# Kernel tuning notes

Measured on AMD Instinct MI355X. Metric: run time of the kernel, lower is better.

The kernel has to match this reference:

```python
import jax, jax.numpy as jnp
import numpy as np
from jax import lax

N, M, B = 512, 1024, 1024  # signal dim, atoms, batch (batch==m required by X = W @ Gamma)
POWER_ITER = 100
IHT_ITER = 50


def setup_inputs() -> dict:
    key = jax.random.key(0)
    k1, k2 = jax.random.split(key)
    Y = jax.random.normal(k1, (B, N), dtype=jnp.float32)
    W = jax.random.normal(k2, (N, M), dtype=jnp.float32)
    return {"Y": Y, "W": W, "K": 64}


def power_method(W):
    # 100 iterations of X <- X W^T W / ||.||; returns last pre-normalization norm
    # (approx largest eigenvalue of W^T W), matching PowerMethod in the source.
    X0 = jax.random.normal(jax.random.key(42), (1, W.shape[1]), dtype=W.dtype)

    def body(i, carry):
        X, _ = carry
        X2 = (X @ W.T) @ W          # [1, m]
        nm = jnp.linalg.norm(X2)
        return (X2 / nm, nm)

    _, nm = lax.fori_loop(0, POWER_ITER, body, (X0, jnp.asarray(1.0, W.dtype)))
    return nm


def hard_threshold_k(G, K):
    # keep entries strictly larger (in abs) than the (K+1)-th largest per row
    a = jnp.sort(jnp.abs(G), axis=1)[:, ::-1]   # descending per row
    T = a[:, K][:, None]                          # [B, 1]
    return G * (jnp.abs(G) > T).astype(G.dtype)


def reference(Y, W, K):
    # NormDict: column-normalize the dictionary
    W = W / jnp.linalg.norm(W, axis=0)
    c = power_method(W)
    eta = 1.0 / c
    Yn = jnp.linalg.norm(Y)

    # IHT sparse coding
    Gamma = hard_threshold_k(Y @ (eta * W), K)     # [B, m]
    residual = Gamma @ W.T - Y                      # [B, n]

    def step(carry, _):
        Gamma, residual = carry
        Gamma = hard_threshold_k(Gamma - eta * (residual @ W), K)
        residual = Gamma @ W.T - Y
        return (Gamma, residual), jnp.linalg.norm(residual) / Yn

    (Gamma, residual), norms = lax.scan(step, (Gamma, residual), None, length=IHT_ITER)

    X = W @ Gamma  # [n, m] @ [B, m] -> requires B == m, as in the torch source
    return X, Gamma, norms
```

## Files before the change

kernel.cpp:

```cpp
#include <hip/hip_runtime.h>


#define DEV __device__ __forceinline__

constexpr int Nd = 512;
constexpr int Md = 1024;
constexpr int Bd = 1024;
constexpr int Ksp = 64;
constexpr int IHT = 50;

DEV float wave_reduce_f(float v) {
#pragma unroll
  for (int off = 32; off > 0; off >>= 1) v += __shfl_down(v, off);
  return v;
}
DEV double wave_reduce_d(double v) {
#pragma unroll
  for (int off = 32; off > 0; off >>= 1) v += __shfl_down(v, off);
  return v;
}
DEV float rfl_f(float v) {
  return __uint_as_float(__builtin_amdgcn_readfirstlane(__float_as_uint(v)));
}

__global__ void k_zero(double* dacc) {
  int t = threadIdx.x;
  if (t < 51) dacc[t] = 0.0;
}

__global__ __launch_bounds__(256) void k_colnorm(const float* __restrict__ W,
                                                 float* __restrict__ cnorm) {
  int col = blockIdx.x * 256 + threadIdx.x;
  double ss = 0.0;
  for (int i = 0; i < Nd; ++i) {
    float w = W[(size_t)i * Md + col];
    ss = fma((double)w, (double)w, ss);
  }
  cnorm[col] = (float)sqrt(ss);
}

__global__ __launch_bounds__(256) void k_normalize(const float* __restrict__ W,
                                                   const float* __restrict__ cnorm,
                                                   float* __restrict__ Wn) {
  int idx = blockIdx.x * 256 + threadIdx.x;
  Wn[idx] = W[idx] / cnorm[idx & (Md - 1)];
}

__global__ __launch_bounds__(256) void k_yn2(const float* __restrict__ Y,
                                             double* __restrict__ dacc) {
  double s = 0.0;
  for (int i = blockIdx.x * 256 + threadIdx.x; i < Bd * Nd; i += gridDim.x * 256) {
    float y = Y[i];
    s = fma((double)y, (double)y, s);
  }
  s = wave_reduce_d(s);
  __shared__ double red[4];
  int lane = threadIdx.x & 63, wid = threadIdx.x >> 6;
  if (lane == 0) red[wid] = s;
  __syncthreads();
  if (threadIdx.x == 0) atomicAdd(&dacc[0], red[0] + red[1] + red[2] + red[3]);
}

template <int BM, int BN, int TN>
__global__ __launch_bounds__(256) void k_gemm_t(const float* __restrict__ A, int lda, int ta,
                                                const float* __restrict__ B, int ldb, int tb,
                                                float* __restrict__ C, int ldc, int Kd,
                                                float scale) {
  constexpr int AE = 32 * BM / 256;
  constexpr int BE = 32 * BN / 256;
  __shared__ __align__(16) float As[32][BM + 4];
  __shared__ __align__(16) float Bs[32][BN + 4];
  const int tid = threadIdx.x;
  const int tx = tid % (BN / TN), ty = tid / (BN / TN);
  const int m0 = blockIdx.y * BM, n0 = blockIdx.x * BN;
  float ra[AE], rb[BE];
  float acc[4][TN];
#pragma unroll
  for (int i = 0; i < 4; ++i)
#pragma unroll
    for (int j = 0; j < TN; ++j) acc[i][j] = 0.f;

  auto loadA = [&](int k0) {
    if (!ta) {
      const int c = tid & 31, r0 = tid >> 5;
#pragma unroll
      for (int i = 0; i < AE; ++i)
        ra[i] = A[(size_t)(m0 + r0 + i * 8) * lda + (k0 + c)];
    } else {
      const int r = tid % BM, c0 = tid / BM;
#pragma unroll
      for (int i = 0; i < AE; ++i)
        ra[i] = A[(size_t)(k0 + c0 + i * (256 / BM)) * lda + (m0 + r)];
    }
  };
  auto storeA = [&]() {
    if (!ta) {
      const int c = tid & 31, r0 = tid >> 5;
#pragma unroll
      for (int i = 0; i < AE; ++i) As[c][r0 + i * 8] = ra[i];
    } else {
      const int r = tid % BM, c0 = tid / BM;
#pragma unroll
      for (int i = 0; i < AE; ++i) As[c0 + i * (256 / BM)][r] = ra[i];
    }
  };
  auto loadB = [&](int k0) {
    if (!tb) {
      const int c = tid % BN, r0 = tid / BN;
#pragma unroll
      for (int i = 0; i < BE; ++i)
        rb[i] = B[(size_t)(k0 + r0 + i * (256 / BN)) * ldb + (n0 + c)];
    } else {
      const int r = tid & 31, c0 = tid >> 5;
#pragma unroll
      for (int i = 0; i < BE; ++i)
        rb[i] = B[(size_t)(n0 + c0 + i * 8) * ldb + (k0 + r)];
    }
  };
  auto storeB = [&]() {
    if (!tb) {
      const int c = tid % BN, r0 = tid / BN;
#pragma unroll
      for (int i = 0; i < BE; ++i) Bs[r0 + i * (256 / BN)][c] = rb[i];
    } else {
      const int r = tid & 31, c0 = tid >> 5;
#pragma unroll
      for (int i = 0; i < BE; ++i) Bs[r][c0 + i * 8] = rb[i];
    }
  };

  loadA(0);
  loadB(0);
  storeA();
  storeB();
  __syncthreads();
  for (int k0 = 0; k0 < Kd; k0 += 32) {
    const bool more = (k0 + 32) < Kd;
    if (more) { loadA(k0 + 32); loadB(k0 + 32); }
#pragma unroll
    for (int kk = 0; kk < 32; ++kk) {
      const float4 a4 = *(const float4*)&As[kk][ty * 4];
      const float aa[4] = {a4.x, a4.y, a4.z, a4.w};
      float bb[TN];
      if constexpr (TN == 4) {
        const float4 b4 = *(const float4*)&Bs[kk][tx * 4];
        bb[0] = b4.x; bb[1] = b4.y; bb[2] = b4.z; bb[3] = b4.w;
      } else {
        const float2 b2 = *(const float2*)&Bs[kk][tx * 2];
        bb[0] = b2.x; bb[1] = b2.y;
      }
#pragma unroll
      for (int i = 0; i < 4; ++i)
#pragma unroll
        for (int j = 0; j < TN; ++j) acc[i][j] = fmaf(aa[i], bb[j], acc[i][j]);
    }
    if (more) {
      __syncthreads();
      storeA();
      storeB();
      __syncthreads();
    }
  }
#pragma unroll
  for (int i = 0; i < 4; ++i) {
    if constexpr (TN == 4) {
      float4 o;
      o.x = acc[i][0] * scale; o.y = acc[i][1] * scale;
      o.z = acc[i][2] * scale; o.w = acc[i][3] * scale;
      *(float4*)&C[(size_t)(m0 + ty * 4 + i) * ldc + n0 + tx * 4] = o;
    } else {
      float2 o;
      o.x = acc[i][0] * scale; o.y = acc[i][1] * scale;
      *(float2*)&C[(size_t)(m0 + ty * 4 + i) * ldc + n0 + tx * 2] = o;
    }
  }
}

DEV float erfinv_xla(float x) {
  float w = -log1pf(-x * x);
  float p;
  if (w < 5.0f) {
    w = w - 2.5f;
    p = 2.81022636e-08f;
    p = fmaf(p, w, 3.43273939e-07f);
    p = fmaf(p, w, -3.5233877e-06f);
    p = fmaf(p, w, -4.39150654e-06f);
    p = fmaf(p, w, 0.00021858087f);
    p = fmaf(p, w, -0.00125372503f);
    p = fmaf(p, w, -0.00417768164f);
    p = fmaf(p, w, 0.246640727f);
    p = fmaf(p, w, 1.50140941f);
  } else {
    w = sqrtf(w) - 3.0f;
    p = -0.000200214257f;
    p = fmaf(p, w, 0.000100950558f);
    p = fmaf(p, w, 0.00134934322f);
    p = fmaf(p, w, -0.00367342844f);
    p = fmaf(p, w, 0.00573950773f);
    p = fmaf(p, w, -0.0076224613f);
    p = fmaf(p, w, 0.00943887047f);
    p = fmaf(p, w, 1.00167406f);
    p = fmaf(p, w, 2.83297682f);
  }
  return p * x;
}

#define TF_ROUND(r)                                  \
  {                                                  \
    x0 += x1;                                        \
    x1 = (x1 << (r)) | (x1 >> (32 - (r)));           \
    x1 ^= x0;                                        \
  }

__global__ void k_x0(float* __restrict__ X0) {
  unsigned i = threadIdx.x;
  unsigned x0 = i, x1 = i + 512u;
  const unsigned ks0 = 0u, ks1 = 42u, ks2 = 0x1BD11BDAu ^ 42u;
  x0 += ks0; x1 += ks1;
  TF_ROUND(13) TF_ROUND(15) TF_ROUND(26) TF_ROUND(6)  x0 += ks1; x1 += ks2 + 1u;
  TF_ROUND(17) TF_ROUND(29) TF_ROUND(16) TF_ROUND(24) x0 += ks2; x1 += ks0 + 2u;
  TF_ROUND(13) TF_ROUND(15) TF_ROUND(26) TF_ROUND(6)  x0 += ks0; x1 += ks1 + 3u;
  TF_ROUND(17) TF_ROUND(29) TF_ROUND(16) TF_ROUND(24) x0 += ks1; x1 += ks2 + 4u;
  TF_ROUND(13) TF_ROUND(15) TF_ROUND(26) TF_ROUND(6)  x0 += ks2; x1 += ks0 + 5u;
  const float lo = -0.99999994f;
  const float sqrt2 = 1.41421356237f;
  {
    float f = __uint_as_float((x0 >> 9) | 0x3f800000u) - 1.0f;
    float u = fmaxf(lo, f * 2.0f + lo);
    X0[i] = sqrt2 * erfinv_xla(u);
  }
  {
    float f = __uint_as_float((x1 >> 9) | 0x3f800000u) - 1.0f;
    float u = fmaxf(lo, f * 2.0f + lo);
    X0[i + 512] = sqrt2 * erfinv_xla(u);
  }
}

__global__ __launch_bounds__(256) void k_z0(const float* __restrict__ X0,
                                            const float* __restrict__ Wn,
                                            float* __restrict__ vout) {
  const int lane = threadIdx.x & 63, wid = threadIdx.x >> 6;
  const int row = blockIdx.x * 4 + wid;
  const float4* wr = (const float4*)(Wn + (size_t)row * Md);
  const float4* x4 = (const float4*)X0;
  float s = 0.f;
#pragma unroll
  for (int e = 0; e < 4; ++e) {
    const float4 w4 = wr[lane + e * 64];
    const float4 xx = x4[lane + e * 64];
    s = fmaf(w4.x, xx.x, s); s = fmaf(w4.y, xx.y, s);
    s = fmaf(w4.z, xx.z, s); s = fmaf(w4.w, xx.w, s);
  }
  s = wave_reduce_f(s);
  if (lane == 0) vout[row] = s;
}

__global__ __launch_bounds__(256) void k_pmv(const float* __restrict__ Mmat,
                                             const float* __restrict__ vin,
                                             float* __restrict__ vout, float scale) {
  const int lane = threadIdx.x & 63, wid = threadIdx.x >> 6;
  const int row = blockIdx.x * 4 + wid;
  const float4* mr = (const float4*)(Mmat + (size_t)row * Nd);
  const float4* v4 = (const float4*)vin;
  float s = 0.f;
#pragma unroll
  for (int e = 0; e < 2; ++e) {
    const float4 m4 = mr[lane + e * 64];
    const float4 xx = v4[lane + e * 64];
    s = fmaf(m4.x, xx.x, s); s = fmaf(m4.y, xx.y, s);
    s = fmaf(m4.z, xx.z, s); s = fmaf(m4.w, xx.w, s);
  }
  s = wave_reduce_f(s);
  if (lane == 0) vout[row] = s * scale;
}

__global__ __launch_bounds__(512) void k_pfinal(const float* __restrict__ v99,
                                                const float* __restrict__ v100,
                                                float* __restrict__ cbuf) {
  __shared__ double r99[8], r100[8];
  const int t = threadIdx.x, lane = t & 63, wid = t >> 6;
  double a = (double)v99[t]; a *= a;
  double b = (double)v100[t]; b *= b;
  a = wave_reduce_d(a);
  b = wave_reduce_d(b);
  if (lane == 0) { r99[wid] = a; r100[wid] = b; }
  __syncthreads();
  if (t == 0) {
    double n99 = 0.0, n100 = 0.0;
    for (int i = 0; i < 8; ++i) { n99 += r99[i]; n100 += r100[i]; }
    float c = (float)(8.0 * sqrt(n100 / n99));
    cbuf[0] = c;
    cbuf[1] = 1.0f / c;
  }
}

__global__ __launch_bounds__(256) void k_iht_all(
    const float* __restrict__ Q, const float* __restrict__ YW,
    const float* __restrict__ cbuf, float* __restrict__ gdense,
    double* __restrict__ normacc) {
  __shared__ float u[Md];
  __shared__ float yws[Md];
  __shared__ float sval[Ksp];
  __shared__ int sidx[Ksp];
  __shared__ unsigned histbuf[2][4][256];
  __shared__ unsigned wred[4];
  __shared__ unsigned sel_need, sel_prefix;
  __shared__ double dred[4];
  __shared__ int scnt;

  const int t = threadIdx.x;
  const int b = blockIdx.x;
  const int lane = t & 63, wv = t >> 6;
  const float eta = cbuf[1];
  const float4 yw = ((const float4*)(YW + (size_t)b * Md))[t];
  ((float4*)yws)[t] = yw;
#pragma unroll
  for (int e = 0; e < 8; ++e) ((unsigned*)histbuf)[t + e * 256] = 0u;
  const float* Qt = Q + t * 4;

  for (int it = -1; it < IHT; ++it) {
    if (it >= 0) {
      const int cnt = scnt;
      float4 p = make_float4(0.f, 0.f, 0.f, 0.f);
      int k = 0;
      for (; k + 8 <= cnt; k += 8) {
#define GROW(j)                                                        \
        const int id##j = __builtin_amdgcn_readfirstlane(sidx[k + j]); \
        const float g##j = rfl_f(sval[k + j]);                         \
        const float4 q##j = *(const float4*)(Qt + (size_t)id##j * Md);
        GROW(0) GROW(1) GROW(2) GROW(3) GROW(4) GROW(5) GROW(6) GROW(7)
#undef GROW
        p.x = fmaf(g0, q0.x, p.x); p.x = fmaf(g1, q1.x, p.x);
        p.x = fmaf(g2, q2.x, p.x); p.x = fmaf(g3, q3.x, p.x);
        p.x = fmaf(g4, q4.x, p.x); p.x = fmaf(g5, q5.x, p.x);
        p.x = fmaf(g6, q6.x, p.x); p.x = fmaf(g7, q7.x, p.x);
        p.y = fmaf(g0, q0.y, p.y); p.y = fmaf(g1, q1.y, p.y);
        p.y = fmaf(g2, q2.y, p.y); p.y = fmaf(g3, q3.y, p.y);
        p.y = fmaf(g4, q4.y, p.y); p.y = fmaf(g5, q5.y, p.y);
        p.y = fmaf(g6, q6.y, p.y); p.y = fmaf(g7, q7.y, p.y);
        p.z = fmaf(g0, q0.z, p.z); p.z = fmaf(g1, q1.z, p.z);
        p.z = fmaf(g2, q2.z, p.z); p.z = fmaf(g3, q3.z, p.z);
        p.z = fmaf(g4, q4.z, p.z); p.z = fmaf(g5, q5.z, p.z);
        p.z = fmaf(g6, q6.z, p.z); p.z = fmaf(g7, q7.z, p.z);
        p.w = fmaf(g0, q0.w, p.w); p.w = fmaf(g1, q1.w, p.w);
        p.w = fmaf(g2, q2.w, p.w); p.w = fmaf(g3, q3.w, p.w);
        p.w = fmaf(g4, q4.w, p.w); p.w = fmaf(g5, q5.w, p.w);
        p.w = fmaf(g6, q6.w, p.w); p.w = fmaf(g7, q7.w, p.w);
      }
      for (; k < cnt; ++k) {
        const int id = __builtin_amdgcn_readfirstlane(sidx[k]);
        const float g = rfl_f(sval[k]);
        const float4 q = *(const float4*)(Qt + (size_t)id * Md);
        p.x = fmaf(g, q.x, p.x); p.y = fmaf(g, q.y, p.y);
        p.z = fmaf(g, q.z, p.z); p.w = fmaf(g, q.w, p.w);
      }
      ((float4*)u)[t] = p;
      __syncthreads();
      if (it >= 1) {
        double part = 0.0;
        if (t < cnt) {
          const int id = sidx[t];
          part = (double)sval[t] * ((double)u[id] - 2.0 * (double)yws[id]);
        }
        part = wave_reduce_d(part);
        if (lane == 0) dred[wv] = part;
      }
      __syncthreads();
      if (it >= 1 && t == 0)
        atomicAdd(&normacc[it - 1], dred[0] + dred[1] + dred[2] + dred[3]);
      float4 uu;
      uu.x = -(eta * (p.x - yw.x)); uu.y = -(eta * (p.y - yw.y));
      uu.z = -(eta * (p.z - yw.z)); uu.w = -(eta * (p.w - yw.w));
      ((float4*)u)[t] = uu;
      __syncthreads();
      if (t < cnt) u[sidx[t]] += sval[t];
      __syncthreads();
    } else {
      float4 uu;
      uu.x = eta * yw.x; uu.y = eta * yw.y; uu.z = eta * yw.z; uu.w = eta * yw.w;
      ((float4*)u)[t] = uu;
      __syncthreads();
    }

    float vals[4];
    unsigned key[4];
    {
      const float4 mv = ((const float4*)u)[t];
      vals[0] = mv.x; vals[1] = mv.y; vals[2] = mv.z; vals[3] = mv.w;
#pragma unroll
      for (int e = 0; e < 4; ++e) key[e] = __float_as_uint(vals[e]) & 0x7fffffffu;
    }

    unsigned need = Ksp + 1, prefix = 0u, pmask = 0u;
#pragma unroll
    for (int pass = 3; pass >= 0; --pass) {
      const int sh = 8 * pass;
      const int pb = pass & 1;
      unsigned(*hist)[256] = histbuf[pb];
#pragma unroll
      for (int e = 0; e < 4; ++e)
        if ((key[e] & pmask) == prefix) atomicAdd(&hist[wv][(key[e] >> sh) & 255u], 1u);
      __syncthreads();
      unsigned* hz = histbuf[pb ^ 1][wv];
      hz[lane] = 0u; hz[lane + 64] = 0u; hz[lane + 128] = 0u; hz[lane + 192] = 0u;
      if (wv == 0) {
        const unsigned c0 = hist[0][lane] + hist[1][lane] + hist[2][lane] + hist[3][lane];
        const unsigned c1 = hist[0][lane + 64] + hist[1][lane + 64] + hist[2][lane + 64] + hist[3][lane + 64];
        const unsigned c2 = hist[0][lane + 128] + hist[1][lane + 128] + hist[2][lane + 128] + hist[3][lane + 128];
        const unsigned c3 = hist[0][lane + 192] + hist[1][lane + 192] + hist[2][lane + 192] + hist[3][lane + 192];
        unsigned s0 = c0, s1 = c1, s2 = c2, s3 = c3;
#pragma unroll
        for (int off = 1; off < 64; off <<= 1) {
          const unsigned y0 = __shfl_down(s0, off), y1 = __shfl_down(s1, off);
          const unsigned y2 = __shfl_down(s2, off), y3 = __shfl_down(s3, off);
          if (lane + off < 64) { s0 += y0; s1 += y1; s2 += y2; s3 += y3; }
        }
        const unsigned T1 = __builtin_amdgcn_readfirstlane(s1);
        const unsigned T2 = __builtin_amdgcn_readfirstlane(s2);
        const unsigned T3 = __builtin_amdgcn_readfirstlane(s3);
        const unsigned i0 = s0 + T1 + T2 + T3;
        const unsigned i1 = s1 + T2 + T3;
        const unsigned i2 = s2 + T3;
        const unsigned i3 = s3;
        if (i0 >= need && i0 - c0 < need) { sel_prefix = prefix | ((unsigned)lane << sh); sel_need = need - (i0 - c0); }
        if (i1 >= need && i1 - c1 < need) { sel_prefix = prefix | ((unsigned)(lane + 64) << sh); sel_need = need - (i1 - c1); }
        if (i2 >= need && i2 - c2 < need) { sel_prefix = prefix | ((unsigned)(lane + 128) << sh); sel_need = need - (i2 - c2); }
        if (i3 >= need && i3 - c3 < need) { sel_prefix = prefix | ((unsigned)(lane + 192) << sh); sel_need = need - (i3 - c3); }
      }
      __syncthreads();
      prefix = sel_prefix;
      need = sel_need;
      pmask |= (255u << sh);
    }
    const unsigned Tbits = prefix;

    unsigned keep = 0u;
    unsigned myc = 0u;
#pragma unroll
    for (int e = 0; e < 4; ++e)
      if (key[e] > Tbits) { keep |= (1u << e); ++myc; }
    unsigned x = myc;
#pragma unroll
    for (int off = 1; off < 64; off <<= 1) {
      const unsigned y = __shfl_up(x, off);
      if (lane >= off) x += y;
    }
    if (lane == 63) wred[wv] = x;
    __syncthreads();
    unsigned addlo = 0u;
    for (int w2 = 0; w2 < wv; ++w2) addlo += wred[w2];
    int base = (int)(x + addlo) - (int)myc;
#pragma unroll
    for (int e = 0; e < 4; ++e) {
      if (keep & (1u << e)) {
        sidx[base] = t * 4 + e;
        sval[base] = vals[e];
        ++base;
      }
    }
    if (t == 0) scnt = (int)(wred[0] + wred[1] + wred[2] + wred[3]);
    if (it == IHT - 1) {
      float4 g;
      g.x = (keep & 1u) ? vals[0] : 0.f;
      g.y = (keep & 2u) ? vals[1] : 0.f;
      g.z = (keep & 4u) ? vals[2] : 0.f;
      g.w = (keep & 8u) ? vals[3] : 0.f;
      ((float4*)(gdense + (size_t)b * Md))[t] = g;
    }
    __syncthreads();
  }

  const int cnt = scnt;
  if (wv == 0) {
    double part = 0.0;
    if (lane < cnt) {
      const int id = sidx[lane];
      float acc2 = 0.f;
      for (int k = 0; k < cnt; ++k)
        acc2 = fmaf(sval[k], Q[(size_t)sidx[k] * Md + id], acc2);
      part = (double)sval[lane] * ((double)acc2 - 2.0 * (double)yws[id]);
    }
    part = wave_reduce_d(part);
    if (lane == 0) atomicAdd(&normacc[IHT - 1], part);
  }
}

__global__ void k_wnorms(const double* __restrict__ dacc, float* __restrict__ onorms) {
  const int t = threadIdx.x;
  if (t < IHT) {
    const double yn2 = dacc[0];
    double r2 = yn2 + dacc[1 + t];
    if (r2 < 0.0) r2 = 0.0;
    onorms[t] = (float)(sqrt(r2) / sqrt(yn2));
  }
}

extern "C" void kernel_launch(void* const* d_in, const int* in_sizes, int n_in,
                              void* d_out, int out_size, void* d_ws, size_t ws_size,
                              hipStream_t stream) {
  (void)in_sizes; (void)n_in; (void)out_size; (void)ws_size;
  const float* Y = (const float*)d_in[0];
  const float* W = (const float*)d_in[1];
  float* out = (float*)d_out;
  float* outX = out;
  float* outG = out + Nd * Md;
  float* outN = outG + Bd * Md;

  char* wsb = (char*)d_ws;
  double* dacc = (double*)wsb;
  float* cbuf = (float*)(wsb + 512);
  float* Wn = (float*)(wsb + 1024);
  float* Q = Wn + Nd * Md;
  float* YW = Q + Md * Md;
  float* Smat = YW + Bd * Md;
  float* S2 = Smat + Nd * Nd;
  float* cnorm = S2 + Nd * Nd;
  float* X0 = cnorm + Md;
  float* V = X0 + Md;

  k_zero<<<1, 64, 0, stream>>>(dacc);
  k_colnorm<<<4, 256, 0, stream>>>(W, cnorm);
  k_normalize<<<2048, 256, 0, stream>>>(W, cnorm, Wn);

  k_gemm_t<64, 32, 2><<<dim3(16, 8), 256, 0, stream>>>(Wn, Md, 0, Wn, Md, 1, Smat, Nd, Md, 1.0f);
  k_gemm_t<64, 32, 2><<<dim3(16, 8), 256, 0, stream>>>(Smat, Nd, 0, Smat, Nd, 0, S2, Nd, Nd, 0.015625f);
  k_gemm_t<64, 64, 4><<<dim3(16, 16), 256, 0, stream>>>(Wn, Md, 1, Wn, Md, 0, Q, Md, Nd, 1.0f);
  k_gemm_t<64, 64, 4><<<dim3(16, 16), 256, 0, stream>>>(Y, Nd, 0, Wn, Md, 0, YW, Md, Nd, 1.0f);
  k_yn2<<<128, 256, 0, stream>>>(Y, dacc);

  k_x0<<<1, 512, 0, stream>>>(X0);
  k_z0<<<128, 256, 0, stream>>>(X0, Wn, V);
  float* pin = V;
  float* pout = V + 512;
  for (int i = 0; i < 49; ++i) {
    k_pmv<<<128, 256, 0, stream>>>(S2, pin, pout, 1.0f);
    float* tp = pin; pin = pout; pout = tp;
  }
  k_pmv<<<128, 256, 0, stream>>>(Smat, pin, V + 1024, 0.125f);
  k_pmv<<<128, 256, 0, stream>>>(Smat, V + 1024, V + 1536, 0.125f);
  k_pfinal<<<1, 512, 0, stream>>>(V + 1024, V + 1536, cbuf);

  k_iht_all<<<1024, 256, 0, stream>>>(Q, YW, cbuf, outG, dacc + 1);
  k_wnorms<<<1, 64, 0, stream>>>(dacc, outN);

  k_gemm_t<64, 32, 2><<<dim3(32, 8), 256, 0, stream>>>(Wn, Md, 0, outG, Md, 0, outX, Md, Md, 1.0f);
}
```

Baseline: 983.2 us.

## Fuse power-method launches into one persistent kernel with grid barriers

Replaces the ~53 separate power-iteration kernel launches (x0 gen, z0, 49 S2 matvecs, two Smat matvecs, final norm) with one persistent kernel of 32 blocks. Each block caches its 16 rows of S2 in LDS and synchronises with the others through flag-based grid barriers. The goal is to remove per-launch overhead and repeated global reads of S2. It relies on all 32 blocks being co-resident and on atomic visibility of the vector exchanges between iterations.

```diff
diff --git a/kernel.cpp b/kernel.cpp
--- a/kernel.cpp
+++ b/kernel.cpp
@@ -9,6 +9,9 @@
 constexpr int Ksp = 64;
 constexpr int IHT = 50;
 
+constexpr int PB = 32;
+constexpr int PRB = Nd / PB;
+
 DEV float wave_reduce_f(float v) {
 #pragma unroll
   for (int off = 32; off > 0; off >>= 1) v += __shfl_down(v, off);
@@ -23,9 +26,10 @@
   return __uint_as_float(__builtin_amdgcn_readfirstlane(__float_as_uint(v)));
 }
 
-__global__ void k_zero(double* dacc) {
+__global__ void k_zero(double* dacc, unsigned* flags) {
   int t = threadIdx.x;
   if (t < 51) dacc[t] = 0.0;
+  if (t >= 64 && t < 64 + PB) flags[t - 64] = 0u;
 }
 
 __global__ __launch_bounds__(256) void k_colnorm(const float* __restrict__ W,
@@ -212,85 +216,154 @@
     x1 ^= x0;                                        \
   }
 
-__global__ void k_x0(float* __restrict__ X0) {
-  unsigned i = threadIdx.x;
-  unsigned x0 = i, x1 = i + 512u;
-  const unsigned ks0 = 0u, ks1 = 42u, ks2 = 0x1BD11BDAu ^ 42u;
-  x0 += ks0; x1 += ks1;
-  TF_ROUND(13) TF_ROUND(15) TF_ROUND(26) TF_ROUND(6)  x0 += ks1; x1 += ks2 + 1u;
-  TF_ROUND(17) TF_ROUND(29) TF_ROUND(16) TF_ROUND(24) x0 += ks2; x1 += ks0 + 2u;
-  TF_ROUND(13) TF_ROUND(15) TF_ROUND(26) TF_ROUND(6)  x0 += ks0; x1 += ks1 + 3u;
-  TF_ROUND(17) TF_ROUND(29) TF_ROUND(16) TF_ROUND(24) x0 += ks1; x1 += ks2 + 4u;
-  TF_ROUND(13) TF_ROUND(15) TF_ROUND(26) TF_ROUND(6)  x0 += ks2; x1 += ks0 + 5u;
-  const float lo = -0.99999994f;
-  const float sqrt2 = 1.41421356237f;
+
+DEV void grid_bar(unsigned* flags, unsigned gen) {
+  __syncthreads();
+  if (threadIdx.x == 0)
+    __hip_atomic_store(&flags[blockIdx.x], gen, __ATOMIC_RELEASE,
+                       __HIP_MEMORY_SCOPE_AGENT);
+  if (threadIdx.x < PB) {
+    while (__hip_atomic_load(&flags[threadIdx.x], __ATOMIC_ACQUIRE,
+                             __HIP_MEMORY_SCOPE_AGENT) < gen)
+      __builtin_amdgcn_s_sleep(1);
+  }
+  __syncthreads();
+}
+
+DEV void v_store(float* p, float v) {
+  __hip_atomic_store(p, v, __ATOMIC_RELAXED, __HIP_MEMORY_SCOPE_AGENT);
+}
+DEV float v_load(const float* p) {
+  return __hip_atomic_load(p, __ATOMIC_RELAXED, __HIP_MEMORY_SCOPE_AGENT);
+}
+
+__global__ __launch_bounds__(512) void k_power_all(
+    const float* __restrict__ Wn, const float* __restrict__ Smat,
+    const float* __restrict__ S2, float* __restrict__ cbuf,
+    float* __restrict__ vbuf, unsigned* __restrict__ flags) {
+  __shared__ __align__(16) float s2s[PRB][Nd];
+  __shared__ __align__(16) float vin_s[Nd];
+  __shared__ __align__(16) float x0s[Md];
+  __shared__ double r99[8], r100[8];
+
+  const int t = threadIdx.x;
+  const int b = blockIdx.x;
+  const int lane = t & 63, wv = t >> 6;
+  unsigned gen = 0;
+
+  float* vA = vbuf;
+  float* vB = vbuf + 512;
+  float* v99 = vbuf + 1024;
+  float* v100 = vbuf + 1536;
+
   {
-    float f = __uint_as_float((x0 >> 9) | 0x3f800000u) - 1.0f;
-    float u = fmaxf(lo, f * 2.0f + lo);
-    X0[i] = sqrt2 * erfinv_xla(u);
+    unsigned i = (unsigned)t;
+    unsigned x0 = i, x1 = i + 512u;
+    const unsigned ks0 = 0u, ks1 = 42u, ks2 = 0x1BD11BDAu ^ 42u;
+    x0 += ks0; x1 += ks1;
+    TF_ROUND(13) TF_ROUND(15) TF_ROUND(26) TF_ROUND(6)  x0 += ks1; x1 += ks2 + 1u;
+    TF_ROUND(17) TF_ROUND(29) TF_ROUND(16) TF_ROUND(24) x0 += ks2; x1 += ks0 + 2u;
+    TF_ROUND(13) TF_ROUND(15) TF_ROUND(26) TF_ROUND(6)  x0 += ks0; x1 += ks1 + 3u;
+    TF_ROUND(17) TF_ROUND(29) TF_ROUND(16) TF_ROUND(24) x0 += ks1; x1 += ks2 + 4u;
+    TF_ROUND(13) TF_ROUND(15) TF_ROUND(26) TF_ROUND(6)  x0 += ks2; x1 += ks0 + 5u;
+    const float lo = -0.99999994f;
+    const float sqrt2 = 1.41421356237f;
+    {
+      float f = __uint_as_float((x0 >> 9) | 0x3f800000u) - 1.0f;
+      float u = fmaxf(lo, f * 2.0f + lo);
+      x0s[t] = sqrt2 * erfinv_xla(u);
+    }
+    {
+      float f = __uint_as_float((x1 >> 9) | 0x3f800000u) - 1.0f;
+      float u = fmaxf(lo, f * 2.0f + lo);
+      x0s[t + 512] = sqrt2 * erfinv_xla(u);
+    }
   }
   {
-    float f = __uint_as_float((x1 >> 9) | 0x3f800000u) - 1.0f;
-    float u = fmaxf(lo, f * 2.0f + lo);
-    X0[i + 512] = sqrt2 * erfinv_xla(u);
-  }
-}
-
-__global__ __launch_bounds__(256) void k_z0(const float* __restrict__ X0,
-                                            const float* __restrict__ Wn,
-                                            float* __restrict__ vout) {
-  const int lane = threadIdx.x & 63, wid = threadIdx.x >> 6;
-  const int row = blockIdx.x * 4 + wid;
-  const float4* wr = (const float4*)(Wn + (size_t)row * Md);
-  const float4* x4 = (const float4*)X0;
-  float s = 0.f;
-#pragma unroll
-  for (int e = 0; e < 4; ++e) {
-    const float4 w4 = wr[lane + e * 64];
-    const float4 xx = x4[lane + e * 64];
-    s = fmaf(w4.x, xx.x, s); s = fmaf(w4.y, xx.y, s);
-    s = fmaf(w4.z, xx.z, s); s = fmaf(w4.w, xx.w, s);
-  }
-  s = wave_reduce_f(s);
-  if (lane == 0) vout[row] = s;
-}
-
-__global__ __launch_bounds__(256) void k_pmv(const float* __restrict__ Mmat,
-                                             const float* __restrict__ vin,
-                                             float* __restrict__ vout, float scale) {
-  const int lane = threadIdx.x & 63, wid = threadIdx.x >> 6;
-  const int row = blockIdx.x * 4 + wid;
-  const float4* mr = (const float4*)(Mmat + (size_t)row * Nd);
-  const float4* v4 = (const float4*)vin;
-  float s = 0.f;
-#pragma unroll
-  for (int e = 0; e < 2; ++e) {
-    const float4 m4 = mr[lane + e * 64];
-    const float4 xx = v4[lane + e * 64];
-    s = fmaf(m4.x, xx.x, s); s = fmaf(m4.y, xx.y, s);
-    s = fmaf(m4.z, xx.z, s); s = fmaf(m4.w, xx.w, s);
-  }
-  s = wave_reduce_f(s);
-  if (lane == 0) vout[row] = s * scale;
-}
-
-__global__ __launch_bounds__(512) void k_pfinal(const float* __restrict__ v99,
-                                                const float* __restrict__ v100,
-                                                float* __restrict__ cbuf) {
-  __shared__ double r99[8], r100[8];
-  const int t = threadIdx.x, lane = t & 63, wid = t >> 6;
-  double a = (double)v99[t]; a *= a;
-  double b = (double)v100[t]; b *= b;
-  a = wave_reduce_d(a);
-  b = wave_reduce_d(b);
-  if (lane == 0) { r99[wid] = a; r100[wid] = b; }
+    const float4* src = (const float4*)(S2 + (size_t)(b * PRB) * Nd);
+    float4* dst = (float4*)&s2s[0][0];
+#pragma unroll
+    for (int i = 0; i < PRB * (Nd / 4) / 512; ++i) dst[t + i * 512] = src[t + i * 512];
+  }
   __syncthreads();
-  if (t == 0) {
-    double n99 = 0.0, n100 = 0.0;
-    for (int i = 0; i < 8; ++i) { n99 += r99[i]; n100 += r100[i]; }
-    float c = (float)(8.0 * sqrt(n100 / n99));
-    cbuf[0] = c;
-    cbuf[1] = 1.0f / c;
+
+  for (int r = wv; r < PRB; r += 8) {
+    const int row = b * PRB + r;
+    const float4* wr = (const float4*)(Wn + (size_t)row * Md);
+    const float4* x4 = (const float4*)x0s;
+    float s = 0.f;
+#pragma unroll
+    for (int e = 0; e < 4; ++e) {
+      const float4 w4 = wr[lane + e * 64];
+      const float4 xx = x4[lane + e * 64];
+      s = fmaf(w4.x, xx.x, s); s = fmaf(w4.y, xx.y, s);
+      s = fmaf(w4.z, xx.z, s); s = fmaf(w4.w, xx.w, s);
+    }
+    s = wave_reduce_f(s);
+    if (lane == 0) v_store(&vA[row], s);
+  }
+  grid_bar(flags, ++gen);
+
+  const float* src = vA;
+  float* dst = vB;
+  for (int itp = 0; itp < 49; ++itp) {
+    vin_s[t] = v_load(&src[t & (Nd - 1)]);
+    __syncthreads();
+    for (int r = wv; r < PRB; r += 8) {
+      const int row = b * PRB + r;
+      const float4* mr = (const float4*)&s2s[r][0];
+      const float4* v4 = (const float4*)vin_s;
+      float s = 0.f;
+#pragma unroll
+      for (int e = 0; e < 2; ++e) {
+        const float4 m4 = mr[lane + e * 64];
+        const float4 xx = v4[lane + e * 64];
+        s = fmaf(m4.x, xx.x, s); s = fmaf(m4.y, xx.y, s);
+        s = fmaf(m4.z, xx.z, s); s = fmaf(m4.w, xx.w, s);
+      }
+      s = wave_reduce_f(s);
+      if (lane == 0) v_store(&dst[row], s);
+    }
+    grid_bar(flags, ++gen);
+    float* tp = (float*)src; src = dst; dst = tp;
+  }
+  for (int ph = 0; ph < 2; ++ph) {
+    const float* vsrc = (ph == 0) ? src : v99;
+    float* vdst = (ph == 0) ? v99 : v100;
+    vin_s[t] = v_load(&vsrc[t & (Nd - 1)]);
+    __syncthreads();
+    for (int r = wv; r < PRB; r += 8) {
+      const int row = b * PRB + r;
+      const float4* mr = (const float4*)(Smat + (size_t)row * Nd);
+      const float4* v4 = (const float4*)vin_s;
+      float s = 0.f;
+#pragma unroll
+      for (int e = 0; e < 2; ++e) {
+        const float4 m4 = mr[lane + e * 64];
+        const float4 xx = v4[lane + e * 64];
+        s = fmaf(m4.x, xx.x, s); s = fmaf(m4.y, xx.y, s);
+        s = fmaf(m4.z, xx.z, s); s = fmaf(m4.w, xx.w, s);
+      }
+      s = wave_reduce_f(s);
+      if (lane == 0) v_store(&vdst[row], s * 0.125f);
+    }
+    grid_bar(flags, ++gen);
+  }
+
+  if (b == 0) {
+    double a = (double)v_load(&v99[t]); a *= a;
+    double bb2 = (double)v_load(&v100[t]); bb2 *= bb2;
+    a = wave_reduce_d(a);
+    bb2 = wave_reduce_d(bb2);
+    if (lane == 0) { r99[wv] = a; r100[wv] = bb2; }
+    __syncthreads();
+    if (t == 0) {
+      double n99 = 0.0, n100 = 0.0;
+      for (int i = 0; i < 8; ++i) { n99 += r99[i]; n100 += r100[i]; }
+      float c = (float)(8.0 * sqrt(n100 / n99));
+      cbuf[0] = c;
+      cbuf[1] = 1.0f / c;
+    }
   }
 }
 
@@ -517,8 +590,9 @@
   float* cnorm = S2 + Nd * Nd;
   float* X0 = cnorm + Md;
   float* V = X0 + Md;
-
-  k_zero<<<1, 64, 0, stream>>>(dacc);
+  unsigned* flags = (unsigned*)(V + 2048);
+
+  k_zero<<<1, 128, 0, stream>>>(dacc, flags);
   k_colnorm<<<4, 256, 0, stream>>>(W, cnorm);
   k_normalize<<<2048, 256, 0, stream>>>(W, cnorm, Wn);
 
@@ -528,17 +602,7 @@
   k_gemm_t<64, 64, 4><<<dim3(16, 16), 256, 0, stream>>>(Y, Nd, 0, Wn, Md, 0, YW, Md, Nd, 1.0f);
   k_yn2<<<128, 256, 0, stream>>>(Y, dacc);
 
-  k_x0<<<1, 512, 0, stream>>>(X0);
-  k_z0<<<128, 256, 0, stream>>>(X0, Wn, V);
-  float* pin = V;
-  float* pout = V + 512;
-  for (int i = 0; i < 49; ++i) {
-    k_pmv<<<128, 256, 0, stream>>>(S2, pin, pout, 1.0f);
-    float* tp = pin; pin = pout; pout = tp;
-  }
-  k_pmv<<<128, 256, 0, stream>>>(Smat, pin, V + 1024, 0.125f);
-  k_pmv<<<128, 256, 0, stream>>>(Smat, V + 1024, V + 1536, 0.125f);
-  k_pfinal<<<1, 512, 0, stream>>>(V + 1024, V + 1536, cbuf);
+  k_power_all<<<PB, 512, 0, stream>>>(Wn, Smat, S2, cbuf, V, flags);
 
   k_iht_all<<<1024, 256, 0, stream>>>(Q, YW, cbuf, outG, dacc + 1);
   k_wnorms<<<1, 64, 0, stream>>>(dacc, outN);
```

Measured after the change: 1.014 ms. 1.03x slower.
